# Kernel tuning notes

Hardware: AMD Instinct MI355X
Metric: run time of the kernel (lower is better)

Reference implementation:

```python
import jax, jax.numpy as jnp
import numpy as np

N_ITER = 4
D = 768  # word_emb_dim == sent_dim of both CrossAttentionBlocks


def setup_inputs() -> dict:
    key = jax.random.key(0)
    ks = jax.random.split(key, 6)
    N_S, N_F = 16384, 4096
    return {
        "sents_emb": jax.random.normal(ks[0], (N_S, D), jnp.float32),
        "func_embed": jax.random.normal(ks[1], (N_F, D), jnp.float32),
        "Wv_f2s": jax.random.normal(ks[2], (D, D), jnp.float32) * 0.02,
        "bv_f2s": jax.random.normal(ks[3], (D,), jnp.float32) * 0.02,
        "Wv_s2f": jax.random.normal(ks[4], (D, D), jnp.float32) * 0.02,
        "bv_s2f": jax.random.normal(ks[5], (D,), jnp.float32) * 0.02,
    }


def reference(sents_emb, func_embed, Wv_f2s, bv_f2s, Wv_s2f, bv_s2f):
    scale = 1.0 / jnp.sqrt(jnp.asarray(D, sents_emb.dtype))
    sents_hid, func_hid = sents_emb, func_embed
    z = None
    for _ in range(N_ITER):  # small fixed iteration count, sequential dependency
        # func2sent: query=sents_hid, key=func_hid, value=W_v(func_hid)
        func_val = func_hid @ Wv_f2s.T + bv_f2s              # [N_f, D]
        z = scale * (sents_hid @ func_hid.T)                  # [N_s, N_f] logits (returned)
        att = jax.nn.softmax(z, axis=1)
        sents_hid = sents_hid + att @ func_val                # [N_s, D]
        # sent2func: query=func_hid, key=sents_hid, value=W_v(sents_hid)
        sent_val = sents_hid @ Wv_s2f.T + bv_s2f              # [N_s, D]
        z2 = scale * (func_hid @ sents_hid.T)                 # [N_f, N_s]
        func_hid = func_hid + jax.nn.softmax(z2, axis=1) @ sent_val
    return (sents_hid, func_hid, z)
```

## Files before the change

### kernel.cpp

```cpp
#include <hip/hip_runtime.h>
#include <stdint.h>

typedef __attribute__((ext_vector_type(8))) short s16x8;
typedef __attribute__((ext_vector_type(8))) unsigned short u16x8;
typedef __attribute__((ext_vector_type(4))) unsigned short u16x4;
typedef __attribute__((ext_vector_type(4))) float f32x4;

__device__ inline unsigned short f2b(float f){
  unsigned u = __builtin_bit_cast(unsigned, f);
  u = u + 0x7fffu + ((u >> 16) & 1u);
  return (unsigned short)(u >> 16);
}
__device__ inline float b2f(unsigned short h){
  unsigned u = ((unsigned)h) << 16;
  return __builtin_bit_cast(float, u);
}

typedef __attribute__((address_space(1))) const unsigned g_uint;
typedef __attribute__((address_space(3))) unsigned l_uint;

__device__ inline void gload_lds16(const void* g, void* l){
  __builtin_amdgcn_global_load_lds((g_uint*)reinterpret_cast<uintptr_t>(g),
                                   (l_uint*)reinterpret_cast<uintptr_t>(l), 16, 0, 0);
}

#define BARF() { __builtin_amdgcn_s_barrier(); asm volatile("" ::: "memory"); }

__device__ inline unsigned xcd_swizzle(unsigned lin, unsigned tot){
  const unsigned q = tot >> 3;
  return (lin & 7) * q + (lin >> 3);
}

template<int EPI>
__global__ __launch_bounds__(512, 2) void gemm256(
    const unsigned short* __restrict__ A, const unsigned short* __restrict__ B,
    int M, int N, int K, float scale,
    float* __restrict__ Cf, unsigned short* __restrict__ Cb,
    float* __restrict__ lsum)
{
  __shared__ __align__(16) char ldsraw[131072];
  const int tid  = threadIdx.x;
  const int wid  = tid >> 6, lane = tid & 63;
  const int wm   = wid >> 2, wn = wid & 3;

  const unsigned gx = gridDim.x, gy = gridDim.y;
  const unsigned lin = blockIdx.x + gx*blockIdx.y;
  const unsigned w   = xcd_swizzle(lin, gx*gy);
  const int bm = (w / gx) * 256, bn = (w % gx) * 256;

  const int NT = K >> 6;

  f32x4 acc[8][4] = {};

  auto stageA = [&](int T, int halfm){
    const int kb = T << 6;
    char* ldsb = ldsraw + ((T & 1) << 16) + halfm*16384;
    #pragma unroll
    for (int i = 0; i < 2; ++i){
      const int lr  = i*64 + (tid >> 3);
      const int gtr = halfm*64 + ((lr < 64) ? lr : lr + 64);
      const int sc  = ((tid & 7)*8) ^ ((lr & 7)*8);
      gload_lds16(A + (size_t)(bm + gtr)*K + kb + sc, ldsb + i*8192 + tid*16);
    }
  };
  auto stageB = [&](int T, int halfk){
    const int kb = (T << 6) + halfk*32;
    char* ldsb = ldsraw + ((T & 1) << 16) + 32768 + halfk*16384;
    #pragma unroll
    for (int i = 0; i < 2; ++i){
      const int lr = i*128 + (tid >> 2);
      const int sc = ((tid & 3)*8) ^ ((lr & 3)*8);
      gload_lds16(B + (size_t)(bn + lr)*K + kb + sc, ldsb + i*8192 + tid*16);
    }
  };

  const int fr = lane & 15;
  const int fo = (lane >> 4) << 4;
  const int amask = (fr & 7) << 4;
  const int bmask = (fr & 3) << 4;

  auto rdA = [&](const char* ldsS, int mh, int kk, s16x8* af){
    const char* ab = ldsS + mh*16384;
    #pragma unroll
    for (int mf = 0; mf < 4; ++mf){
      const int r = wm*64 + mf*16 + fr;
      af[mf] = *(const s16x8*)(ab + r*128 + ((kk*64 + fo) ^ amask));
    }
  };
  auto rdB = [&](const char* ldsS, int kk, s16x8* bf){
    const char* bb = ldsS + 32768 + kk*16384;
    #pragma unroll
    for (int nf = 0; nf < 4; ++nf){
      const int r = wn*64 + nf*16 + fr;
      bf[nf] = *(const s16x8*)(bb + r*64 + (fo ^ bmask));
    }
  };

  stageB(0, 0); stageA(0, 0); stageA(0, 1); stageB(0, 1);
  stageB(1, 0); stageA(1, 0);
  asm volatile("s_waitcnt vmcnt(4)" ::: "memory");
  BARF();

  for (int T = 0; T < NT; ++T){
    const char* ldsS = ldsraw + ((T & 1) << 16);
    s16x8 af[4], bf[4];
    rdA(ldsS, 0, 0, af); rdB(ldsS, 0, bf);
    if (T + 1 < NT) stageA(T + 1, 1);
    BARF();
    __builtin_amdgcn_s_setprio(1);
    #pragma unroll
    for (int mf = 0; mf < 4; ++mf)
      #pragma unroll
      for (int nf = 0; nf < 4; ++nf)
        acc[mf][nf] = __builtin_amdgcn_mfma_f32_16x16x32_bf16(af[mf], bf[nf], acc[mf][nf], 0, 0, 0);
    __builtin_amdgcn_s_setprio(0);
    BARF();
    rdA(ldsS, 1, 0, af);
    if (T + 1 < NT) stageB(T + 1, 1);
    BARF();
    __builtin_amdgcn_s_setprio(1);
    #pragma unroll
    for (int mf = 0; mf < 4; ++mf)
      #pragma unroll
      for (int nf = 0; nf < 4; ++nf)
        acc[4 + mf][nf] = __builtin_amdgcn_mfma_f32_16x16x32_bf16(af[mf], bf[nf], acc[4 + mf][nf], 0, 0, 0);
    __builtin_amdgcn_s_setprio(0);
    BARF();
    rdA(ldsS, 0, 1, af); rdB(ldsS, 1, bf);
    if (T + 2 < NT) stageB(T + 2, 0);
    BARF();
    __builtin_amdgcn_s_setprio(1);
    #pragma unroll
    for (int mf = 0; mf < 4; ++mf)
      #pragma unroll
      for (int nf = 0; nf < 4; ++nf)
        acc[mf][nf] = __builtin_amdgcn_mfma_f32_16x16x32_bf16(af[mf], bf[nf], acc[mf][nf], 0, 0, 0);
    __builtin_amdgcn_s_setprio(0);
    BARF();
    rdA(ldsS, 1, 1, af);
    if (T + 2 < NT) stageA(T + 2, 0);
    BARF();
    __builtin_amdgcn_s_setprio(1);
    #pragma unroll
    for (int mf = 0; mf < 4; ++mf)
      #pragma unroll
      for (int nf = 0; nf < 4; ++nf)
        acc[4 + mf][nf] = __builtin_amdgcn_mfma_f32_16x16x32_bf16(af[mf], bf[nf], acc[4 + mf][nf], 0, 0, 0);
    __builtin_amdgcn_s_setprio(0);
    if (T < NT - 2) { asm volatile("s_waitcnt vmcnt(4)" ::: "memory"); }
    else           { asm volatile("s_waitcnt vmcnt(0)" ::: "memory"); }
    BARF();
  }

  float* lds_rs = (float*)ldsraw;
  if (tid < 256) lds_rs[tid] = 0.f;
  __syncthreads();

  const int er0 = bm + wm*128 + ((lane >> 4) << 2);
  const int ec0 = bn + wn*64  + (lane & 15);
  #pragma unroll
  for (int mf = 0; mf < 8; ++mf){
    float rs[4] = {0.f, 0.f, 0.f, 0.f};
    #pragma unroll
    for (int nf = 0; nf < 4; ++nf){
      #pragma unroll
      for (int j = 0; j < 4; ++j){
        const int row = er0 + mf*16 + j;
        const int col = ec0 + nf*16;
        const size_t idx = (size_t)row * N + col;
        const float v = acc[mf][nf][j];
        unsigned short eb;
        if (EPI == 5){ eb = f2b(__expf(v * scale)); }
        else { const float zz = v * scale; Cf[idx] = zz; eb = f2b(__expf(zz)); }
        Cb[idx] = eb;
        rs[j] += b2f(eb);
      }
    }
    #pragma unroll
    for (int o = 8; o; o >>= 1){
      #pragma unroll
      for (int j = 0; j < 4; ++j) rs[j] += __shfl_xor(rs[j], o, 64);
    }
    if ((lane & 15) == 0){
      const int rbase = wm*128 + mf*16 + ((lane >> 4) << 2);
      #pragma unroll
      for (int j = 0; j < 4; ++j) atomicAdd(&lds_rs[rbase + j], rs[j]);
    }
  }
  __syncthreads();
  if (tid < 256) atomicAdd(&lsum[bm + tid], lds_rs[tid]);
}

template<int EPI>
__global__ __launch_bounds__(256, 4) void gemm_bt(
    const unsigned short* __restrict__ A, const unsigned short* __restrict__ B,
    int M, int N, int KS, float scale, const float* __restrict__ bias,
    const float* __restrict__ lsum,
    float* __restrict__ Cf, unsigned short* __restrict__ Cb)
{
  __shared__ unsigned short As[128*64];
  __shared__ unsigned short Bs[128*64];
  const int tid  = threadIdx.x;
  const int wid  = tid >> 6, lane = tid & 63;
  const int wr   = wid >> 1, wc = wid & 1;

  const unsigned gx = gridDim.x, gy = gridDim.y;
  const unsigned lin = blockIdx.x + gx*(blockIdx.y + gy*blockIdx.z);
  const unsigned w   = xcd_swizzle(lin, gx*gy*gridDim.z);
  const unsigned bxs = w % gx;
  const unsigned rest = w / gx;
  const unsigned bys = rest % gy;
  const unsigned bzs = rest / gy;

  const int bm   = bys * 128, bn = bxs * 128;
  const int kb   = bzs * KS, ke = kb + KS;

  f32x4 acc[4][4] = {};

  const int l8   = lane >> 3;
  const int scol = ((((lane & 7) << 4) ^ (l8 << 4)) >> 1);
  const int Klead = gridDim.z * KS;

  const unsigned short* Ag[4]; const unsigned short* Bg[4];
  unsigned short* Al[4]; unsigned short* Bl[4];
  #pragma unroll
  for (int i = 0; i < 4; ++i){
    const int row = wid*32 + i*8 + l8;
    Ag[i] = A + (size_t)(bm + row) * Klead + scol;
    Bg[i] = B + (size_t)(bn + row) * Klead + scol;
    Al[i] = As + (wid*4 + i) * 512;
    Bl[i] = Bs + (wid*4 + i) * 512;
  }

  const int fr    = lane & 15;
  const int fk    = (lane >> 4) << 4;
  const int amask = (fr & 7) << 4;

  for (int k0 = kb; k0 < ke; k0 += 64){
    if (k0 != kb) __syncthreads();
    #pragma unroll
    for (int i = 0; i < 4; ++i){
      gload_lds16(Ag[i] + k0, Al[i]);
      gload_lds16(Bg[i] + k0, Bl[i]);
    }
    __syncthreads();
    #pragma unroll
    for (int kk = 0; kk < 2; ++kk){
      s16x8 af[4], bf[4];
      #pragma unroll
      for (int m = 0; m < 4; ++m){
        const int row = (wr << 6) + m*16 + fr;
        const int off = row*128 + (((kk << 6) + fk) ^ amask);
        af[m] = *(const s16x8*)((const char*)As + off);
      }
      #pragma unroll
      for (int n = 0; n < 4; ++n){
        const int row = (wc << 6) + n*16 + fr;
        const int off = row*128 + (((kk << 6) + fk) ^ amask);
        bf[n] = *(const s16x8*)((const char*)Bs + off);
      }
      #pragma unroll
      for (int m = 0; m < 4; ++m)
        #pragma unroll
        for (int n = 0; n < 4; ++n)
          acc[m][n] = __builtin_amdgcn_mfma_f32_16x16x32_bf16(af[m], bf[n], acc[m][n], 0, 0, 0);
    }
  }

  const int gr0 = bm + (wr << 6) + ((lane >> 4) << 2);
  const int gc0 = bn + (wc << 6) + (lane & 15);
  const size_t pbase = (size_t)bzs * M * N;
  #pragma unroll
  for (int m = 0; m < 4; ++m){
    #pragma unroll
    for (int j = 0; j < 4; ++j){
      const int row = gr0 + m*16 + j;
      const float li = (EPI == 7) ? 1.0f / lsum[row] : 0.f;
      #pragma unroll
      for (int n = 0; n < 4; ++n){
        const int col = gc0 + n*16;
        const size_t idx = (size_t)row * N + col;
        const float v = acc[m][n][j];
        if      (EPI == 2) Cb[idx] = f2b(v + bias[row]);
        else if (EPI == 4) Cf[pbase + idx] = v;
        else if (EPI == 7){ const float o = Cf[idx] + li * v; Cf[idx] = o; Cb[idx] = f2b(o); }
      }
    }
  }
}

__global__ __launch_bounds__(256) void reduce_splitk(
    const float* __restrict__ P, int S, size_t stride4,
    const float* __restrict__ lsum, int d4,
    float* __restrict__ Cf, unsigned short* __restrict__ Cb, int n4)
{
  const int i = blockIdx.x * 256 + threadIdx.x;
  if (i >= n4) return;
  f32x4 s = {0.f, 0.f, 0.f, 0.f};
  for (int k = 0; k < S; ++k) s += ((const f32x4*)P)[(size_t)k * stride4 + i];
  const float li = 1.0f / lsum[i / d4];
  f32x4 r = ((const f32x4*)Cf)[i];
  r += s * li;
  ((f32x4*)Cf)[i] = r;
  u16x4 o;
  o[0] = f2b(r[0]); o[1] = f2b(r[1]); o[2] = f2b(r[2]); o[3] = f2b(r[3]);
  ((u16x4*)Cb)[i] = o;
}

__global__ void cvt8(const float* __restrict__ src, float* __restrict__ dstf,
                     unsigned short* __restrict__ dstb, int n8)
{
  const int i = blockIdx.x * 256 + threadIdx.x;
  if (i >= n8) return;
  const f32x4 a = ((const f32x4*)src)[2*i];
  const f32x4 b = ((const f32x4*)src)[2*i + 1];
  if (dstf){ ((f32x4*)dstf)[2*i] = a; ((f32x4*)dstf)[2*i + 1] = b; }
  u16x8 o;
  o[0]=f2b(a[0]); o[1]=f2b(a[1]); o[2]=f2b(a[2]); o[3]=f2b(a[3]);
  o[4]=f2b(b[0]); o[5]=f2b(b[1]); o[6]=f2b(b[2]); o[7]=f2b(b[3]);
  ((u16x8*)dstb)[i] = o;
}

extern "C" void kernel_launch(void* const* d_in, const int* in_sizes, int n_in,
                              void* d_out, int out_size, void* d_ws, size_t ws_size,
                              hipStream_t stream)
{
  (void)in_sizes; (void)n_in; (void)out_size; (void)ws_size;
  const float* sents = (const float*)d_in[0];
  const float* funcs = (const float*)d_in[1];
  const float* WvA   = (const float*)d_in[2];
  const float* bvA   = (const float*)d_in[3];
  const float* WvB   = (const float*)d_in[4];
  const float* bvB   = (const float*)d_in[5];

  const int NS = 16384, NF = 4096, D = 768;

  float* outS = (float*)d_out;
  float* outF = outS + (size_t)NS * D;
  float* outZ = outF + (size_t)NF * D;

  char* ws = (char*)d_ws;
  unsigned short* att = (unsigned short*)ws;  ws += (size_t)NS * NF * 2;
  unsigned short* z2  = att;
  unsigned short* sb  = (unsigned short*)ws;  ws += (size_t)NS * D * 2;
  unsigned short* fb  = (unsigned short*)ws;  ws += (size_t)NF * D * 2;
  unsigned short* fvT = (unsigned short*)ws;  ws += (size_t)D * NF * 2;
  unsigned short* svT = (unsigned short*)ws;  ws += (size_t)D * NS * 2;
  unsigned short* wA  = (unsigned short*)ws;  ws += (size_t)D * D * 2;
  unsigned short* wB  = (unsigned short*)ws;  ws += (size_t)D * D * 2;
  float* lsum = (float*)ws;  ws += (size_t)NS * 4;
  float* Pbuf = (float*)ws;  ws += (size_t)NF * D * 4 * 4;

  const float scale = 0.036084391824351615f;

  cvt8<<<dim3((NS*D/8 + 255)/256), 256, 0, stream>>>(sents, outS, sb, NS*D/8);
  cvt8<<<dim3((NF*D/8 + 255)/256), 256, 0, stream>>>(funcs, outF, fb, NF*D/8);
  cvt8<<<dim3((D*D/8 + 255)/256),  256, 0, stream>>>(WvA, nullptr, wA, D*D/8);
  cvt8<<<dim3((D*D/8 + 255)/256),  256, 0, stream>>>(WvB, nullptr, wB, D*D/8);

  for (int it = 0; it < 4; ++it){
    gemm_bt<2><<<dim3(NF/128, D/128, 1), dim3(256), 0, stream>>>(wA, fb, D, NF, D, 0.f, bvA, nullptr, nullptr, fvT);
    hipMemsetAsync(lsum, 0, NS*4, stream);
    if (it < 3){
      gemm256<5><<<dim3(NF/256, NS/256), dim3(512), 0, stream>>>(sb, fb, NS, NF, D, scale, nullptr, att, lsum);
    } else {
      gemm256<6><<<dim3(NF/256, NS/256), dim3(512), 0, stream>>>(sb, fb, NS, NF, D, scale, outZ, att, lsum);
    }
    gemm_bt<7><<<dim3(D/128, NS/128, 1), dim3(256), 0, stream>>>(att, fvT, NS, D, NF, 0.f, nullptr, lsum, outS, sb);
    gemm_bt<2><<<dim3(NS/128, D/128, 1), dim3(256), 0, stream>>>(wB, sb, D, NS, D, 0.f, bvB, nullptr, nullptr, svT);
    hipMemsetAsync(lsum, 0, NF*4, stream);
    gemm256<5><<<dim3(NS/256, NF/256), dim3(512), 0, stream>>>(fb, sb, NF, NS, D, scale, nullptr, z2, lsum);
    gemm_bt<4><<<dim3(D/128, NF/128, 4), dim3(256), 0, stream>>>(z2, svT, NF, D, 4096, 0.f, nullptr, nullptr, Pbuf, nullptr);
    reduce_splitk<<<dim3(NF*D/4/256), 256, 0, stream>>>(Pbuf, 4, (size_t)NF*D/4, lsum, D/4, outF, fb, NF*D/4);
  }
}
```

Measured before the change: 2.190 ms.

## Shrink logits GEMM tile to 256x128 with triple-buffered K=32 pipeline

Reworks the QK^T logits GEMM from a 256x256 tile with double-buffered K=64 stages and four MFMA phases per step into a 256x128 tile. Each K=32 step is staged into one of three LDS buffers, and the loop has a single barrier-separated MFMA phase. LDS drops to 72KB and per-thread accumulators halve, so launch bounds allow more resident blocks and twice as many workgroups are launched. The cost is lower arithmetic intensity per tile, more redundant A-tile loads from global memory, and more epilogue atomics into the row sums.

```diff
diff --git a/kernel.cpp b/kernel.cpp
--- a/kernel.cpp
+++ b/kernel.cpp
@@ -32,80 +32,63 @@
 }
 
 template<int EPI>
-__global__ __launch_bounds__(512, 2) void gemm256(
+__global__ __launch_bounds__(512, 4) void gemm256(
     const unsigned short* __restrict__ A, const unsigned short* __restrict__ B,
     int M, int N, int K, float scale,
     float* __restrict__ Cf, unsigned short* __restrict__ Cb,
     float* __restrict__ lsum)
 {
-  __shared__ __align__(16) char ldsraw[131072];
+  __shared__ __align__(16) char ldsraw[73728];
   const int tid  = threadIdx.x;
   const int wid  = tid >> 6, lane = tid & 63;
-  const int wm   = wid >> 2, wn = wid & 3;
+  const int wm   = wid >> 1, wn = wid & 1;
 
   const unsigned gx = gridDim.x, gy = gridDim.y;
   const unsigned lin = blockIdx.x + gx*blockIdx.y;
   const unsigned w   = xcd_swizzle(lin, gx*gy);
-  const int bm = (w / gx) * 256, bn = (w % gx) * 256;
-
-  const int NT = K >> 6;
-
-  f32x4 acc[8][4] = {};
-
-  auto stageA = [&](int T, int halfm){
-    const int kb = T << 6;
-    char* ldsb = ldsraw + ((T & 1) << 16) + halfm*16384;
-    #pragma unroll
-    for (int i = 0; i < 2; ++i){
-      const int lr  = i*64 + (tid >> 3);
-      const int gtr = halfm*64 + ((lr < 64) ? lr : lr + 64);
-      const int sc  = ((tid & 7)*8) ^ ((lr & 7)*8);
-      gload_lds16(A + (size_t)(bm + gtr)*K + kb + sc, ldsb + i*8192 + tid*16);
-    }
-  };
-  auto stageB = [&](int T, int halfk){
-    const int kb = (T << 6) + halfk*32;
-    char* ldsb = ldsraw + ((T & 1) << 16) + 32768 + halfk*16384;
+  const int bm = (w / gx) * 256, bn = (w % gx) * 128;
+
+  const int NT = K >> 5;
+
+  f32x4 acc[4][4] = {};
+
+  auto stage = [&](int T){
+    char* base = ldsraw + (T % 3) * 24576;
+    const int kb = T << 5;
     #pragma unroll
     for (int i = 0; i < 2; ++i){
       const int lr = i*128 + (tid >> 2);
       const int sc = ((tid & 3)*8) ^ ((lr & 3)*8);
-      gload_lds16(B + (size_t)(bn + lr)*K + kb + sc, ldsb + i*8192 + tid*16);
-    }
+      gload_lds16(A + (size_t)(bm + lr)*K + kb + sc, base + i*8192 + tid*16);
+    }
+    const int lrb = tid >> 2;
+    const int scb = ((tid & 3)*8) ^ ((lrb & 3)*8);
+    gload_lds16(B + (size_t)(bn + lrb)*K + kb + scb, base + 16384 + tid*16);
   };
 
   const int fr = lane & 15;
   const int fo = (lane >> 4) << 4;
-  const int amask = (fr & 7) << 4;
-  const int bmask = (fr & 3) << 4;
-
-  auto rdA = [&](const char* ldsS, int mh, int kk, s16x8* af){
-    const char* ab = ldsS + mh*16384;
+  const int xm = (fr & 3) << 4;
+
+  stage(0); stage(1);
+  asm volatile("s_waitcnt vmcnt(3)" ::: "memory");
+  BARF();
+
+  for (int T = 0; T < NT; ++T){
+    const char* ab = ldsraw + (T % 3) * 24576;
+    const char* bb = ab + 16384;
+    s16x8 af[4], bf[4];
     #pragma unroll
     for (int mf = 0; mf < 4; ++mf){
       const int r = wm*64 + mf*16 + fr;
-      af[mf] = *(const s16x8*)(ab + r*128 + ((kk*64 + fo) ^ amask));
-    }
-  };
-  auto rdB = [&](const char* ldsS, int kk, s16x8* bf){
-    const char* bb = ldsS + 32768 + kk*16384;
+      af[mf] = *(const s16x8*)(ab + r*64 + (fo ^ xm));
+    }
     #pragma unroll
     for (int nf = 0; nf < 4; ++nf){
       const int r = wn*64 + nf*16 + fr;
-      bf[nf] = *(const s16x8*)(bb + r*64 + (fo ^ bmask));
-    }
-  };
-
-  stageB(0, 0); stageA(0, 0); stageA(0, 1); stageB(0, 1);
-  stageB(1, 0); stageA(1, 0);
-  asm volatile("s_waitcnt vmcnt(4)" ::: "memory");
-  BARF();
-
-  for (int T = 0; T < NT; ++T){
-    const char* ldsS = ldsraw + ((T & 1) << 16);
-    s16x8 af[4], bf[4];
-    rdA(ldsS, 0, 0, af); rdB(ldsS, 0, bf);
-    if (T + 1 < NT) stageA(T + 1, 1);
+      bf[nf] = *(const s16x8*)(bb + r*64 + (fo ^ xm));
+    }
+    if (T + 2 < NT) stage(T + 2);
     BARF();
     __builtin_amdgcn_s_setprio(1);
     #pragma unroll
@@ -114,41 +97,8 @@
       for (int nf = 0; nf < 4; ++nf)
         acc[mf][nf] = __builtin_amdgcn_mfma_f32_16x16x32_bf16(af[mf], bf[nf], acc[mf][nf], 0, 0, 0);
     __builtin_amdgcn_s_setprio(0);
-    BARF();
-    rdA(ldsS, 1, 0, af);
-    if (T + 1 < NT) stageB(T + 1, 1);
-    BARF();
-    __builtin_amdgcn_s_setprio(1);
-    #pragma unroll
-    for (int mf = 0; mf < 4; ++mf)
-      #pragma unroll
-      for (int nf = 0; nf < 4; ++nf)
-        acc[4 + mf][nf] = __builtin_amdgcn_mfma_f32_16x16x32_bf16(af[mf], bf[nf], acc[4 + mf][nf], 0, 0, 0);
-    __builtin_amdgcn_s_setprio(0);
-    BARF();
-    rdA(ldsS, 0, 1, af); rdB(ldsS, 1, bf);
-    if (T + 2 < NT) stageB(T + 2, 0);
-    BARF();
-    __builtin_amdgcn_s_setprio(1);
-    #pragma unroll
-    for (int mf = 0; mf < 4; ++mf)
-      #pragma unroll
-      for (int nf = 0; nf < 4; ++nf)
-        acc[mf][nf] = __builtin_amdgcn_mfma_f32_16x16x32_bf16(af[mf], bf[nf], acc[mf][nf], 0, 0, 0);
-    __builtin_amdgcn_s_setprio(0);
-    BARF();
-    rdA(ldsS, 1, 1, af);
-    if (T + 2 < NT) stageA(T + 2, 0);
-    BARF();
-    __builtin_amdgcn_s_setprio(1);
-    #pragma unroll
-    for (int mf = 0; mf < 4; ++mf)
-      #pragma unroll
-      for (int nf = 0; nf < 4; ++nf)
-        acc[4 + mf][nf] = __builtin_amdgcn_mfma_f32_16x16x32_bf16(af[mf], bf[nf], acc[4 + mf][nf], 0, 0, 0);
-    __builtin_amdgcn_s_setprio(0);
-    if (T < NT - 2) { asm volatile("s_waitcnt vmcnt(4)" ::: "memory"); }
-    else           { asm volatile("s_waitcnt vmcnt(0)" ::: "memory"); }
+    if (T < NT - 2) { asm volatile("s_waitcnt vmcnt(3)" ::: "memory"); }
+    else            { asm volatile("s_waitcnt vmcnt(0)" ::: "memory"); }
     BARF();
   }
 
@@ -156,10 +106,10 @@
   if (tid < 256) lds_rs[tid] = 0.f;
   __syncthreads();
 
-  const int er0 = bm + wm*128 + ((lane >> 4) << 2);
-  const int ec0 = bn + wn*64  + (lane & 15);
+  const int er0 = bm + wm*64 + ((lane >> 4) << 2);
+  const int ec0 = bn + wn*64 + (lane & 15);
   #pragma unroll
-  for (int mf = 0; mf < 8; ++mf){
+  for (int mf = 0; mf < 4; ++mf){
     float rs[4] = {0.f, 0.f, 0.f, 0.f};
     #pragma unroll
     for (int nf = 0; nf < 4; ++nf){
@@ -182,7 +132,7 @@
       for (int j = 0; j < 4; ++j) rs[j] += __shfl_xor(rs[j], o, 64);
     }
     if ((lane & 15) == 0){
-      const int rbase = wm*128 + mf*16 + ((lane >> 4) << 2);
+      const int rbase = wm*64 + mf*16 + ((lane >> 4) << 2);
       #pragma unroll
       for (int j = 0; j < 4; ++j) atomicAdd(&lds_rs[rbase + j], rs[j]);
     }
@@ -362,14 +312,14 @@
     gemm_bt<2><<<dim3(NF/128, D/128, 1), dim3(256), 0, stream>>>(wA, fb, D, NF, D, 0.f, bvA, nullptr, nullptr, fvT);
     hipMemsetAsync(lsum, 0, NS*4, stream);
     if (it < 3){
-      gemm256<5><<<dim3(NF/256, NS/256), dim3(512), 0, stream>>>(sb, fb, NS, NF, D, scale, nullptr, att, lsum);
+      gemm256<5><<<dim3(NF/128, NS/256), dim3(512), 0, stream>>>(sb, fb, NS, NF, D, scale, nullptr, att, lsum);
     } else {
-      gemm256<6><<<dim3(NF/256, NS/256), dim3(512), 0, stream>>>(sb, fb, NS, NF, D, scale, outZ, att, lsum);
+      gemm256<6><<<dim3(NF/128, NS/256), dim3(512), 0, stream>>>(sb, fb, NS, NF, D, scale, outZ, att, lsum);
     }
     gemm_bt<7><<<dim3(D/128, NS/128, 1), dim3(256), 0, stream>>>(att, fvT, NS, D, NF, 0.f, nullptr, lsum, outS, sb);
     gemm_bt<2><<<dim3(NS/128, D/128, 1), dim3(256), 0, stream>>>(wB, sb, D, NS, D, 0.f, bvB, nullptr, nullptr, svT);
     hipMemsetAsync(lsum, 0, NF*4, stream);
-    gemm256<5><<<dim3(NS/256, NF/256), dim3(512), 0, stream>>>(fb, sb, NF, NS, D, scale, nullptr, z2, lsum);
+    gemm256<5><<<dim3(NS/128, NF/256), dim3(512), 0, stream>>>(fb, sb, NF, NS, D, scale, nullptr, z2, lsum);
     gemm_bt<4><<<dim3(D/128, NF/128, 4), dim3(256), 0, stream>>>(z2, svT, NF, D, 4096, 0.f, nullptr, nullptr, Pbuf, nullptr);
     reduce_splitk<<<dim3(NF*D/4/256), 256, 0, stream>>>(Pbuf, 4, (size_t)NF*D/4, lsum, D/4, outF, fb, NF*D/4);
   }
```

Result: slower. 2.255 ms (+3.0%).

## Stage GEMM epilogues through LDS for vectorized coalesced global stores

Applied to the files above, without the earlier changes.

Both GEMM kernels now write their accumulator fragments into per-wave swizzled LDS scratch and read them back as contiguous row vectors. This lets the bf16 exp output, fp32 partials and residual updates go out as 16-byte vector stores instead of scattered 2- or 4-byte stores. In gemm256 the row sums are also computed from the staged vectors with fewer shuffles and LDS atomics. The cost is extra LDS traffic and a barrier before the epilogue. The fr variable used in gemm256 must already be in scope from earlier code.

```diff
diff --git a/kernel.cpp b/kernel.cpp
--- a/kernel.cpp
+++ b/kernel.cpp
@@ -25,6 +25,7 @@
 }
 
 #define BARF() { __builtin_amdgcn_s_barrier(); asm volatile("" ::: "memory"); }
+#define LGKM0() { asm volatile("s_waitcnt lgkmcnt(0)" ::: "memory"); }
 
 __device__ inline unsigned xcd_swizzle(unsigned lin, unsigned tot){
   const unsigned q = tot >> 3;
@@ -148,44 +149,55 @@
         acc[4 + mf][nf] = __builtin_amdgcn_mfma_f32_16x16x32_bf16(af[mf], bf[nf], acc[4 + mf][nf], 0, 0, 0);
     __builtin_amdgcn_s_setprio(0);
     if (T < NT - 2) { asm volatile("s_waitcnt vmcnt(4)" ::: "memory"); }
-    else           { asm volatile("s_waitcnt vmcnt(0)" ::: "memory"); }
-    BARF();
-  }
-
+    else            { asm volatile("s_waitcnt vmcnt(0)" ::: "memory"); }
+    BARF();
+  }
+
+  char* wlds = ldsraw + wid*16384;
+  const int hi = lane >> 4;
+  #pragma unroll
+  for (int mf = 0; mf < 8; ++mf){
+    #pragma unroll
+    for (int j = 0; j < 4; ++j){
+      const int rl = mf*16 + hi*4 + j;
+      #pragma unroll
+      for (int nf = 0; nf < 4; ++nf){
+        const float zz = acc[mf][nf][j] * scale;
+        if (EPI == 6){
+          const int row = bm + wm*128 + rl;
+          const int col = bn + wn*64 + fr + nf*16;
+          Cf[(size_t)row * N + col] = zz;
+        }
+        const int cl = fr + nf*16;
+        *(unsigned short*)(wlds + rl*128 + ((cl*2) ^ (((rl>>2)&3) << 5))) = f2b(__expf(zz));
+      }
+    }
+  }
+  LGKM0();
+
+  float rs16[16];
+  const int g8 = lane >> 3;
+  #pragma unroll
+  for (int t = 0; t < 16; ++t){
+    const u16x8 v = *(const u16x8*)(wlds + t*1024 + lane*16);
+    const int rl = t*8 + g8;
+    const int c0 = (((lane & 7)*16) ^ (((rl>>2)&3) << 5)) >> 1;
+    const int row = bm + wm*128 + rl;
+    *(u16x8*)(Cb + (size_t)row * N + bn + wn*64 + c0) = v;
+    float s = 0.f;
+    #pragma unroll
+    for (int k = 0; k < 8; ++k) s += b2f(v[k]);
+    s += __shfl_xor(s, 1, 64); s += __shfl_xor(s, 2, 64); s += __shfl_xor(s, 4, 64);
+    rs16[t] = s;
+  }
+  __syncthreads();
   float* lds_rs = (float*)ldsraw;
   if (tid < 256) lds_rs[tid] = 0.f;
   __syncthreads();
-
-  const int er0 = bm + wm*128 + ((lane >> 4) << 2);
-  const int ec0 = bn + wn*64  + (lane & 15);
-  #pragma unroll
-  for (int mf = 0; mf < 8; ++mf){
-    float rs[4] = {0.f, 0.f, 0.f, 0.f};
-    #pragma unroll
-    for (int nf = 0; nf < 4; ++nf){
-      #pragma unroll
-      for (int j = 0; j < 4; ++j){
-        const int row = er0 + mf*16 + j;
-        const int col = ec0 + nf*16;
-        const size_t idx = (size_t)row * N + col;
-        const float v = acc[mf][nf][j];
-        unsigned short eb;
-        if (EPI == 5){ eb = f2b(__expf(v * scale)); }
-        else { const float zz = v * scale; Cf[idx] = zz; eb = f2b(__expf(zz)); }
-        Cb[idx] = eb;
-        rs[j] += b2f(eb);
-      }
-    }
-    #pragma unroll
-    for (int o = 8; o; o >>= 1){
-      #pragma unroll
-      for (int j = 0; j < 4; ++j) rs[j] += __shfl_xor(rs[j], o, 64);
-    }
-    if ((lane & 15) == 0){
-      const int rbase = wm*128 + mf*16 + ((lane >> 4) << 2);
-      #pragma unroll
-      for (int j = 0; j < 4; ++j) atomicAdd(&lds_rs[rbase + j], rs[j]);
-    }
+  if ((lane & 7) == 0){
+    #pragma unroll
+    for (int t = 0; t < 16; ++t)
+      atomicAdd(&lds_rs[wm*128 + t*8 + g8], rs16[t]);
   }
   __syncthreads();
   if (tid < 256) atomicAdd(&lsum[bm + tid], lds_rs[tid]);
@@ -198,8 +210,9 @@
     const float* __restrict__ lsum,
     float* __restrict__ Cf, unsigned short* __restrict__ Cb)
 {
-  __shared__ unsigned short As[128*64];
-  __shared__ unsigned short Bs[128*64];
+  __shared__ __align__(16) char ldsb[32768];
+  unsigned short* As = (unsigned short*)ldsb;
+  unsigned short* Bs = As + 128*64;
   const int tid  = threadIdx.x;
   const int wid  = tid >> 6, lane = tid & 63;
   const int wr   = wid >> 1, wc = wid & 1;
@@ -266,26 +279,50 @@
           acc[m][n] = __builtin_amdgcn_mfma_f32_16x16x32_bf16(af[m], bf[n], acc[m][n], 0, 0, 0);
     }
   }
-
-  const int gr0 = bm + (wr << 6) + ((lane >> 4) << 2);
-  const int gc0 = bn + (wc << 6) + (lane & 15);
+  __syncthreads();
+
+  char* wlds = ldsb + wid*8192;
+  const int hi = lane >> 4;
   const size_t pbase = (size_t)bzs * M * N;
   #pragma unroll
-  for (int m = 0; m < 4; ++m){
-    #pragma unroll
-    for (int j = 0; j < 4; ++j){
-      const int row = gr0 + m*16 + j;
-      const float li = (EPI == 7) ? 1.0f / lsum[row] : 0.f;
-      #pragma unroll
-      for (int n = 0; n < 4; ++n){
-        const int col = gc0 + n*16;
-        const size_t idx = (size_t)row * N + col;
-        const float v = acc[m][n][j];
-        if      (EPI == 2) Cb[idx] = f2b(v + bias[row]);
-        else if (EPI == 4) Cf[pbase + idx] = v;
-        else if (EPI == 7){ const float o = Cf[idx] + li * v; Cf[idx] = o; Cb[idx] = f2b(o); }
+  for (int mh = 0; mh < 2; ++mh){
+    #pragma unroll
+    for (int ms = 0; ms < 2; ++ms){
+      #pragma unroll
+      for (int j = 0; j < 4; ++j){
+        const int rl = ms*16 + hi*4 + j;
+        #pragma unroll
+        for (int n = 0; n < 4; ++n){
+          const int cl = fr + n*16;
+          *(float*)(wlds + rl*256 + ((cl*4) ^ (((rl>>2)&3) << 5))) = acc[mh*2 + ms][n][j];
+        }
       }
     }
+    LGKM0();
+    #pragma unroll
+    for (int t = 0; t < 8; ++t){
+      const f32x4 d = *(const f32x4*)(wlds + t*1024 + lane*16);
+      const int rl = t*4 + hi;
+      const int c0 = (((lane & 15)*16) ^ (((rl>>2)&3) << 5)) >> 2;
+      const int row = bm + (wr << 6) + mh*32 + rl;
+      const int col = bn + (wc << 6) + c0;
+      const size_t idx = (size_t)row * N + col;
+      if (EPI == 2){
+        const float bi = bias[row];
+        u16x4 o; o[0]=f2b(d[0]+bi); o[1]=f2b(d[1]+bi); o[2]=f2b(d[2]+bi); o[3]=f2b(d[3]+bi);
+        *(u16x4*)(Cb + idx) = o;
+      } else if (EPI == 4){
+        *(f32x4*)(Cf + pbase + idx) = d;
+      } else {
+        const float li = 1.0f / lsum[row];
+        f32x4 o = *(const f32x4*)(Cf + idx);
+        o += d * li;
+        *(f32x4*)(Cf + idx) = o;
+        u16x4 ob; ob[0]=f2b(o[0]); ob[1]=f2b(o[1]); ob[2]=f2b(o[2]); ob[3]=f2b(o[3]);
+        *(u16x4*)(Cb + idx) = ob;
+      }
+    }
+    LGKM0();
   }
 }
 
```

Result: no change. 2.196 ms (+0.2%).
